# Kernel optimization log

Hardware: AMD Instinct MI355X
Metric: run time of the kernel (lower is better)

The kernel has to match this reference:

```python
import jax, jax.numpy as jnp
import numpy as np
from jax import lax

EPS = 1e-5

def setup_inputs() -> dict:
    key = jax.random.key(0)
    ks = jax.random.split(key, 9)
    B, C, O, H, W = 2, 64, 64, 192, 192
    x = jax.random.normal(ks[0], (B, C, H, W), jnp.float32)
    dw_w = jax.random.normal(ks[1], (C, 1, 3, 3), jnp.float32) * (1.0 / 3.0)
    dw_b = jax.random.normal(ks[2], (C,), jnp.float32) * 0.1
    bn_g = jnp.ones((C,), jnp.float32)
    bn_b = jnp.zeros((C,), jnp.float32)
    bn_m = jax.random.normal(ks[3], (C,), jnp.float32) * 0.1
    bn_v = jax.random.uniform(ks[4], (C,), jnp.float32, 0.5, 1.5)
    # small pointwise weights -> moderate offsets (module inits these to 0)
    pw_w = jax.random.normal(ks[5], (27, C), jnp.float32) * 0.05
    pw_b = jax.random.normal(ks[6], (27,), jnp.float32) * 0.05
    dcn_w = jax.random.normal(ks[7], (O, C, 3, 3), jnp.float32) * (1.0 / np.sqrt(C * 9))
    dcn_b = jax.random.normal(ks[8], (O,), jnp.float32) * 0.1
    return {"x": x, "dw_w": dw_w, "dw_b": dw_b, "bn_g": bn_g, "bn_b": bn_b,
            "bn_m": bn_m, "bn_v": bn_v, "pw_w": pw_w, "pw_b": pw_b,
            "dcn_w": dcn_w, "dcn_b": dcn_b}


def _dcnv2_forward(x, dw_w, dw_b, bn_g, bn_b, bn_m, bn_v, pw_w, pw_b, dcn_w, dcn_b):
    B, C, H, W = x.shape
    O = dcn_w.shape[0]
    K = 9  # 3x3 kernel positions

    # --- offset/mask head: depthwise 3x3 conv + BN(eval) + ReLU + 1x1 conv ---
    h = lax.conv_general_dilated(x, dw_w, (1, 1), ((1, 1), (1, 1)),
                                 feature_group_count=C,
                                 dimension_numbers=("NCHW", "OIHW", "NCHW"))
    h = h + dw_b[None, :, None, None]
    h = (h - bn_m[None, :, None, None]) * lax.rsqrt(bn_v + EPS)[None, :, None, None]
    h = h * bn_g[None, :, None, None] + bn_b[None, :, None, None]
    h = jax.nn.relu(h)
    om = jnp.einsum("bchw,oc->bohw", h, pw_w) + pw_b[None, :, None, None]  # [B,27,H,W]

    off = om[:, :18].reshape(B, K, 2, H, W)  # torchvision layout: (dy, dx) per kernel pos
    dy, dx = off[:, :, 0], off[:, :, 1]      # [B,K,H,W]
    mask = jax.nn.sigmoid(om[:, 18:])        # [B,K,H,W]

    # --- deformable sampling positions ---
    kk = jnp.arange(K)
    ry = (kk // 3 - 1).astype(x.dtype)[None, :, None, None]
    rx = (kk % 3 - 1).astype(x.dtype)[None, :, None, None]
    iy = jnp.arange(H, dtype=x.dtype)[None, None, :, None]
    ix = jnp.arange(W, dtype=x.dtype)[None, None, None, :]
    py = iy + ry + dy  # [B,K,H,W]
    px = ix + rx + dx

    y0 = jnp.floor(py)
    x0 = jnp.floor(px)
    wy1 = py - y0
    wx1 = px - x0
    wy0 = 1.0 - wy1
    wx0 = 1.0 - wx1

    x_flat = x.reshape(B, C, H * W)

    def gather(yi, xi):
        # zero-padded gather at integer coords yi, xi [B,K,H,W] -> [B,C,K,H,W]
        valid = (yi >= 0) & (yi < H) & (xi >= 0) & (xi < W)
        yc = jnp.clip(yi, 0, H - 1).astype(jnp.int32)
        xc = jnp.clip(xi, 0, W - 1).astype(jnp.int32)
        idx = (yc * W + xc).reshape(B, 1, K * H * W)
        v = jnp.take_along_axis(x_flat, idx, axis=2).reshape(B, C, K, H, W)
        return v * valid.astype(x.dtype)[:, None]

    val = (gather(y0, x0) * (wy0 * wx0)[:, None]
           + gather(y0, x0 + 1) * (wy0 * wx1)[:, None]
           + gather(y0 + 1, x0) * (wy1 * wx0)[:, None]
           + gather(y0 + 1, x0 + 1) * (wy1 * wx1)[:, None])  # [B,C,K,H,W]

    val = val * mask[:, None]  # DCNv2 modulation
    out = jnp.einsum("bckhw,ock->bohw", val, dcn_w.reshape(O, C, K))
    out = out + dcn_b[None, :, None, None]

    # --- InstanceNorm2d (affine=False) + ReLU ---
    mu = out.mean(axis=(2, 3), keepdims=True)
    var = out.var(axis=(2, 3), keepdims=True)
    out = (out - mu) * lax.rsqrt(var + EPS)
    return jax.nn.relu(out)


def reference(x, dw_w, dw_b, bn_g, bn_b, bn_m, bn_v, pw_w, pw_b, dcn_w, dcn_b):
    return _dcnv2_forward(x, dw_w, dw_b, bn_g, bn_b, bn_m, bn_v, pw_w, pw_b, dcn_w, dcn_b)
```

## Files before the change

kernel.cpp:

```cpp
#include <hip/hip_runtime.h>
#include <math.h>

#define H_ 192
#define W_ 192
#define HW_ 36864
#define C_ 64
#define O_ 64
#define B_ 2
#define K_ 9
#define EPS_ 1e-5f

typedef __attribute__((ext_vector_type(8))) short short8;
typedef __attribute__((ext_vector_type(4))) float f32x4;

__device__ __forceinline__ unsigned int f2bf(float f) {
  unsigned int u = __float_as_uint(f);
  u += 0x7FFFu + ((u >> 16) & 1u);
  return u >> 16;
}
__device__ __forceinline__ unsigned int pk2bf(float lo, float hi) {
  return f2bf(lo) | (f2bf(hi) << 16);
}
__device__ __forceinline__ void acc8(const uint4 u, const float g, float* v) {
  v[0] = fmaf(g, __uint_as_float(u.x << 16), v[0]);
  v[1] = fmaf(g, __uint_as_float(u.x & 0xFFFF0000u), v[1]);
  v[2] = fmaf(g, __uint_as_float(u.y << 16), v[2]);
  v[3] = fmaf(g, __uint_as_float(u.y & 0xFFFF0000u), v[3]);
  v[4] = fmaf(g, __uint_as_float(u.z << 16), v[4]);
  v[5] = fmaf(g, __uint_as_float(u.z & 0xFFFF0000u), v[5]);
  v[6] = fmaf(g, __uint_as_float(u.w << 16), v[6]);
  v[7] = fmaf(g, __uint_as_float(u.w & 0xFFFF0000u), v[7]);
}

__global__ __launch_bounds__(256) void k1_dw(const float* __restrict__ x,
                                             const float* __restrict__ dw_w,
                                             const float* __restrict__ dw_b,
                                             const float* __restrict__ bn_g,
                                             const float* __restrict__ bn_b,
                                             const float* __restrict__ bn_m,
                                             const float* __restrict__ bn_v,
                                             float* __restrict__ h) {
  const int plane = blockIdx.y;
  const int c = plane & (C_ - 1);
  const int p = blockIdx.x * 256 + threadIdx.x;
  const int y = p / W_;
  const int xx = p - y * W_;
  const float* xp = x + (size_t)plane * HW_;
  float w[9];
#pragma unroll
  for (int i = 0; i < 9; ++i) w[i] = dw_w[c * 9 + i];
  float s = 0.f;
#pragma unroll
  for (int dy = 0; dy < 3; ++dy) {
    const int yy = y + dy - 1;
    if (yy < 0 || yy >= H_) continue;
#pragma unroll
    for (int dx = 0; dx < 3; ++dx) {
      const int xc = xx + dx - 1;
      if (xc < 0 || xc >= W_) continue;
      s = fmaf(w[dy * 3 + dx], xp[yy * W_ + xc], s);
    }
  }
  const float scale = bn_g[c] * rsqrtf(bn_v[c] + EPS_);
  const float shift = fmaf(dw_b[c] - bn_m[c], scale, bn_b[c]);
  h[(size_t)plane * HW_ + p] = fmaxf(fmaf(s, scale, shift), 0.f);
}

__global__ __launch_bounds__(256) void k1b_t(const float* __restrict__ x,
                                             unsigned short* __restrict__ xR) {
  const int b = blockIdx.y;
  const int p = blockIdx.x * 256 + threadIdx.x;
  const int y = p / W_;
  const int xx = p - y * W_;
  const float* xp = x + (size_t)b * C_ * HW_ + p;
  uint4* dst = (uint4*)xR + (size_t)b * HW_ * 8;
#pragma unroll
  for (int cc = 0; cc < 8; ++cc) {
    uint4 u;
    u.x = pk2bf(xp[(size_t)(cc * 8 + 0) * HW_], xp[(size_t)(cc * 8 + 1) * HW_]);
    u.y = pk2bf(xp[(size_t)(cc * 8 + 2) * HW_], xp[(size_t)(cc * 8 + 3) * HW_]);
    u.z = pk2bf(xp[(size_t)(cc * 8 + 4) * HW_], xp[(size_t)(cc * 8 + 5) * HW_]);
    u.w = pk2bf(xp[(size_t)(cc * 8 + 6) * HW_], xp[(size_t)(cc * 8 + 7) * HW_]);
    dst[(y * 8 + cc) * W_ + xx] = u;
  }
}

__global__ __launch_bounds__(256) void k2_pw(const float* __restrict__ h,
                                             const float* __restrict__ pw_w,
                                             const float* __restrict__ pw_b,
                                             float* __restrict__ om) {
  __shared__ float wl[C_ * 28];
  const int b = blockIdx.y;
  const int p = blockIdx.x * 256 + threadIdx.x;
  for (int i = threadIdx.x; i < C_ * 28; i += 256) {
    const int c = i / 28, j = i - c * 28;
    wl[i] = (j < 27) ? pw_w[j * C_ + c] : 0.f;
  }
  __syncthreads();
  float s[27];
#pragma unroll
  for (int j = 0; j < 27; ++j) s[j] = 0.f;
  const float* hp = h + (size_t)b * C_ * HW_ + p;
  for (int c = 0; c < C_; ++c) {
    const float hv = hp[(size_t)c * HW_];
    float wv[28];
#pragma unroll
    for (int q = 0; q < 7; ++q)
      *(float4*)&wv[q * 4] = *(const float4*)&wl[c * 28 + q * 4];
#pragma unroll
    for (int j = 0; j < 27; ++j) s[j] = fmaf(hv, wv[j], s[j]);
  }
  float* op = om + (size_t)b * 27 * HW_ + p;
#pragma unroll
  for (int j = 0; j < 27; ++j) op[(size_t)j * HW_] = s[j] + pw_b[j];
}

__global__ __launch_bounds__(256) void k0_wt(const float* __restrict__ dcn_w,
                                             unsigned short* __restrict__ wT2) {
  const int i = blockIdx.x * 256 + threadIdx.x;
  const int o = i / (C_ * 9);
  const int rem = i - o * (C_ * 9);
  const int c = rem / 9;
  const int kk = rem - c * 9;
  wT2[((size_t)(kk * O_) + o) * C_ + c] = (unsigned short)f2bf(dcn_w[i]);
}

__global__ __launch_bounds__(256, 4) void k3_dcn(const unsigned short* __restrict__ xR,
                                                 const float* __restrict__ om,
                                                 const unsigned short* __restrict__ wT2,
                                                 float* __restrict__ pre,
                                                 float* __restrict__ pstats2) {
  __shared__ __align__(16) unsigned short smem[8192];
  unsigned short* wlds = smem;
  unsigned short* vlds = smem + 4096;

  const int tid = threadIdx.x;
  const int t = (blockIdx.x & 7) * 144 + (blockIdx.x >> 3);
  const int b = t / 576;
  const int p0 = (t - b * 576) * 64;
  const uint4* xr = (const uint4*)xR + (size_t)b * HW_ * 8;
  const float* omb = om + (size_t)b * 27 * HW_;

  const int pxi = tid & 63;
  const int cq = tid >> 6;
  const int lr = pxi & 15;
  const int lg = pxi >> 4;
  const int oo0 = cq * 16;

  const int p = p0 + pxi;
  const int y = p / W_;
  const int xx = p - y * W_;

  f32x4 acc[4];
#pragma unroll
  for (int j = 0; j < 4; ++j) acc[j] = (f32x4){0.f, 0.f, 0.f, 0.f};

  for (int k = 0; k < K_; ++k) {
    const uint4* wsrc = (const uint4*)(wT2 + (k << 12));
    const uint4 wv0 = wsrc[tid];
    const uint4 wv1 = wsrc[tid + 256];
    const float dyv = omb[(size_t)(2 * k) * HW_ + p];
    const float dxv = omb[(size_t)(2 * k + 1) * HW_ + p];
    float mk = omb[(size_t)(18 + k) * HW_ + p];
    mk = 1.f / (1.f + __expf(-mk));
    const int ky = k / 3;
    const int kx = k - ky * 3;
    const float py = (float)(y + ky - 1) + dyv;
    const float pxf = (float)(xx + kx - 1) + dxv;
    const float y0f = floorf(py), x0f = floorf(pxf);
    const float wy1 = py - y0f, wx1 = pxf - x0f;
    const float wy0 = 1.f - wy1, wx0 = 1.f - wx1;
    const int y0 = (int)y0f, x0i = (int)x0f;
    const int y1 = y0 + 1, x1i = x0i + 1;
    const bool vy0 = (y0 >= 0) & (y0 < H_);
    const bool vy1 = (y1 >= 0) & (y1 < H_);
    const bool vx0 = (x0i >= 0) & (x0i < W_);
    const bool vx1 = (x1i >= 0) & (x1i < W_);
    const int yc0 = min(max(y0, 0), H_ - 1), yc1 = min(max(y1, 0), H_ - 1);
    const int xc0 = min(max(x0i, 0), W_ - 1), xc1 = min(max(x1i, 0), W_ - 1);
    const float g0 = (vy0 & vx0) ? wy0 * wx0 * mk : 0.f;
    const float g1 = (vy0 & vx1) ? wy0 * wx1 * mk : 0.f;
    const float g2 = (vy1 & vx0) ? wy1 * wx0 * mk : 0.f;
    const float g3 = (vy1 & vx1) ? wy1 * wx1 * mk : 0.f;

    const int ry0 = yc0 * (8 * W_), ry1 = yc1 * (8 * W_);
    const int ca = cq * W_, cb = (cq + 4) * W_;
    const uint4 a0 = xr[ry0 + ca + xc0], b0v = xr[ry0 + cb + xc0];
    const uint4 a1 = xr[ry0 + ca + xc1], b1v = xr[ry0 + cb + xc1];
    const uint4 a2 = xr[ry1 + ca + xc0], b2v = xr[ry1 + cb + xc0];
    const uint4 a3 = xr[ry1 + ca + xc1], b3v = xr[ry1 + cb + xc1];
    float val[16];
#pragma unroll
    for (int i = 0; i < 16; ++i) val[i] = 0.f;
    acc8(a0, g0, val);  acc8(b0v, g0, val + 8);
    acc8(a1, g1, val);  acc8(b1v, g1, val + 8);
    acc8(a2, g2, val);  acc8(b2v, g2, val + 8);
    acc8(a3, g3, val);  acc8(b3v, g3, val + 8);

    __syncthreads();
    {
      const int r0 = tid >> 3, b0i = tid & 7;
      ((uint4*)wlds)[(r0 << 3) + (b0i ^ (r0 & 7))] = wv0;
      const int r1 = (tid + 256) >> 3;
      ((uint4*)wlds)[(r1 << 3) + (b0i ^ (r1 & 7))] = wv1;
    }
    {
      uint4 pka, pkb;
      pka.x = pk2bf(val[0], val[1]);
      pka.y = pk2bf(val[2], val[3]);
      pka.z = pk2bf(val[4], val[5]);
      pka.w = pk2bf(val[6], val[7]);
      pkb.x = pk2bf(val[8], val[9]);
      pkb.y = pk2bf(val[10], val[11]);
      pkb.z = pk2bf(val[12], val[13]);
      pkb.w = pk2bf(val[14], val[15]);
      const int rsw = pxi & 7;
      ((uint4*)vlds)[(pxi << 3) + (cq ^ rsw)] = pka;
      ((uint4*)vlds)[(pxi << 3) + ((cq + 4) ^ rsw)] = pkb;
    }
    __syncthreads();
#pragma unroll
    for (int ks = 0; ks < 2; ++ks) {
      const int kb = (ks << 2) + lg;
      const int ra = oo0 + lr;
      const short8 afr = *(const short8*)&((const uint4*)wlds)[(ra << 3) + (kb ^ (ra & 7))];
#pragma unroll
      for (int j = 0; j < 4; ++j) {
        const int rb = (j << 4) + lr;
        const short8 bfr = *(const short8*)&((const uint4*)vlds)[(rb << 3) + (kb ^ (rb & 7))];
        acc[j] = __builtin_amdgcn_mfma_f32_16x16x32_bf16(afr, bfr, acc[j], 0, 0, 0);
      }
    }
  }

#pragma unroll
  for (int q = 0; q < 4; ++q) {
    float s = acc[0][q] + acc[1][q] + acc[2][q] + acc[3][q];
    float s2 = fmaf(acc[0][q], acc[0][q],
               fmaf(acc[1][q], acc[1][q],
               fmaf(acc[2][q], acc[2][q], acc[3][q] * acc[3][q])));
#pragma unroll
    for (int m = 1; m < 16; m <<= 1) {
      s += __shfl_xor(s, m);
      s2 += __shfl_xor(s2, m);
    }
    if (lr == 0) {
      const int pll = oo0 + (lg << 2) + q;
      ((float2*)pstats2)[(size_t)t * 64 + pll] = make_float2(s, s2);
    }
  }

  __syncthreads();
  float* fsm = (float*)smem;
#pragma unroll
  for (int j = 0; j < 4; ++j)
#pragma unroll
    for (int q = 0; q < 4; ++q)
      fsm[(oo0 + (lg << 2) + q) * 64 + (j << 4) + lr] = acc[j][q];
  __syncthreads();
  {
    const float4* fsm4 = (const float4*)fsm;
    float* prebase = pre + (size_t)b * O_ * HW_ + p0;
#pragma unroll
    for (int i = 0; i < 4; ++i) {
      const int f = tid + (i << 8);
      const int o = f >> 4;
      const int px4 = (f & 15) << 2;
      *(float4*)&prebase[(size_t)o * HW_ + px4] = fsm4[f];
    }
  }
}

__global__ __launch_bounds__(256) void k4_fin(const float* __restrict__ pstats2,
                                              float* __restrict__ stats) {
  const int pl = blockIdx.x;
  const int b = pl >> 6, o = pl & 63;
  const float2* src = (const float2*)pstats2 + (size_t)b * 576 * 64 + o;
  float s = 0.f, s2 = 0.f;
  for (int tt = threadIdx.x; tt < 576; tt += 256) {
    const float2 v = src[(size_t)tt * 64];
    s += v.x;
    s2 += v.y;
  }
#pragma unroll
  for (int m = 1; m < 64; m <<= 1) {
    s += __shfl_xor(s, m);
    s2 += __shfl_xor(s2, m);
  }
  __shared__ float ls[4], ls2[4];
  const int wid = threadIdx.x >> 6;
  if ((threadIdx.x & 63) == 0) { ls[wid] = s; ls2[wid] = s2; }
  __syncthreads();
  if (threadIdx.x == 0) {
    const float ts = ls[0] + ls[1] + ls[2] + ls[3];
    const float ts2 = ls2[0] + ls2[1] + ls2[2] + ls2[3];
    const float inv = 1.f / (float)HW_;
    const float mu = ts * inv;
    const float var = fmaxf(fmaf(-mu, mu, ts2 * inv), 0.f);
    stats[pl * 2] = mu;
    stats[pl * 2 + 1] = rsqrtf(var + EPS_);
  }
}

__global__ __launch_bounds__(256) void k5_norm(const float* __restrict__ pre,
                                               const float* __restrict__ stats,
                                               float* __restrict__ out) {
  const int i4 = blockIdx.x * 256 + threadIdx.x;
  const int plane = i4 / 9216;
  const float mu = stats[plane * 2];
  const float rs = stats[plane * 2 + 1];
  float4 v = ((const float4*)pre)[i4];
  v.x = fmaxf((v.x - mu) * rs, 0.f);
  v.y = fmaxf((v.y - mu) * rs, 0.f);
  v.z = fmaxf((v.z - mu) * rs, 0.f);
  v.w = fmaxf((v.w - mu) * rs, 0.f);
  ((float4*)out)[i4] = v;
}

extern "C" void kernel_launch(void* const* d_in, const int* in_sizes, int n_in,
                              void* d_out, int out_size, void* d_ws, size_t ws_size,
                              hipStream_t stream) {
  const float* x = (const float*)d_in[0];
  const float* dw_w = (const float*)d_in[1];
  const float* dw_b = (const float*)d_in[2];
  const float* bn_g = (const float*)d_in[3];
  const float* bn_b = (const float*)d_in[4];
  const float* bn_m = (const float*)d_in[5];
  const float* bn_v = (const float*)d_in[6];
  const float* pw_w = (const float*)d_in[7];
  const float* pw_b = (const float*)d_in[8];
  const float* dcn_w = (const float*)d_in[9];
  float* out = (float*)d_out;

  float* ws = (float*)d_ws;
  float* h = ws;
  float* om = h + (size_t)B_ * C_ * HW_;
  unsigned short* wT2 = (unsigned short*)(om + (size_t)B_ * 27 * HW_);
  float* stats = (float*)(wT2 + (size_t)K_ * O_ * C_);
  if (ws_size < (size_t)(4718592 + 1990656 + 18432 + 256) * sizeof(float)) return;
  float* pre = h;
  unsigned short* xR = (unsigned short*)d_out;
  float* pstats2 = (float*)d_out + 2359296;

  k0_wt<<<dim3(144), dim3(256), 0, stream>>>(dcn_w, wT2);
  k1b_t<<<dim3(HW_ / 256, B_), dim3(256), 0, stream>>>(x, xR);
  k1_dw<<<dim3(HW_ / 256, B_ * C_), dim3(256), 0, stream>>>(x, dw_w, dw_b, bn_g, bn_b,
                                                            bn_m, bn_v, h);
  k2_pw<<<dim3(HW_ / 256, B_), dim3(256), 0, stream>>>(h, pw_w, pw_b, om);
  k3_dcn<<<dim3(B_ * HW_ / 64), dim3(256), 0, stream>>>(xR, om, wT2, pre, pstats2);
  k4_fin<<<dim3(B_ * O_), dim3(256), 0, stream>>>(pstats2, stats);
  k5_norm<<<dim3(B_ * O_ * HW_ / 4 / 256), dim3(256), 0, stream>>>(pre, stats, out);
}
```

Baseline: 106.7 us.

## Switch DCN sampling and MFMA to fp16, pack offsets/mask as float4

```diff
diff --git a/kernel.cpp b/kernel.cpp
--- a/kernel.cpp
+++ b/kernel.cpp
@@ -1,4 +1,5 @@
 #include <hip/hip_runtime.h>
+#include <hip/hip_fp16.h>
 #include <math.h>
 
 #define H_ 192
@@ -10,26 +11,14 @@
 #define K_ 9
 #define EPS_ 1e-5f
 
-typedef __attribute__((ext_vector_type(8))) short short8;
+typedef __attribute__((ext_vector_type(8))) _Float16 f16x8;
 typedef __attribute__((ext_vector_type(4))) float f32x4;
 
-__device__ __forceinline__ unsigned int f2bf(float f) {
-  unsigned int u = __float_as_uint(f);
-  u += 0x7FFFu + ((u >> 16) & 1u);
-  return u >> 16;
-}
-__device__ __forceinline__ unsigned int pk2bf(float lo, float hi) {
-  return f2bf(lo) | (f2bf(hi) << 16);
-}
-__device__ __forceinline__ void acc8(const uint4 u, const float g, float* v) {
-  v[0] = fmaf(g, __uint_as_float(u.x << 16), v[0]);
-  v[1] = fmaf(g, __uint_as_float(u.x & 0xFFFF0000u), v[1]);
-  v[2] = fmaf(g, __uint_as_float(u.y << 16), v[2]);
-  v[3] = fmaf(g, __uint_as_float(u.y & 0xFFFF0000u), v[3]);
-  v[4] = fmaf(g, __uint_as_float(u.z << 16), v[4]);
-  v[5] = fmaf(g, __uint_as_float(u.z & 0xFFFF0000u), v[5]);
-  v[6] = fmaf(g, __uint_as_float(u.w << 16), v[6]);
-  v[7] = fmaf(g, __uint_as_float(u.w & 0xFFFF0000u), v[7]);
+union U16B { uint4 u; __half2 h[4]; };
+
+__device__ __forceinline__ unsigned int pkh(float lo, float hi) {
+  return (unsigned int)__half_as_ushort(__float2half(lo)) |
+         ((unsigned int)__half_as_ushort(__float2half(hi)) << 16);
 }
 
 __global__ __launch_bounds__(256) void k1_dw(const float* __restrict__ x,
@@ -77,10 +66,10 @@
 #pragma unroll
   for (int cc = 0; cc < 8; ++cc) {
     uint4 u;
-    u.x = pk2bf(xp[(size_t)(cc * 8 + 0) * HW_], xp[(size_t)(cc * 8 + 1) * HW_]);
-    u.y = pk2bf(xp[(size_t)(cc * 8 + 2) * HW_], xp[(size_t)(cc * 8 + 3) * HW_]);
-    u.z = pk2bf(xp[(size_t)(cc * 8 + 4) * HW_], xp[(size_t)(cc * 8 + 5) * HW_]);
-    u.w = pk2bf(xp[(size_t)(cc * 8 + 6) * HW_], xp[(size_t)(cc * 8 + 7) * HW_]);
+    u.x = pkh(xp[(size_t)(cc * 8 + 0) * HW_], xp[(size_t)(cc * 8 + 1) * HW_]);
+    u.y = pkh(xp[(size_t)(cc * 8 + 2) * HW_], xp[(size_t)(cc * 8 + 3) * HW_]);
+    u.z = pkh(xp[(size_t)(cc * 8 + 4) * HW_], xp[(size_t)(cc * 8 + 5) * HW_]);
+    u.w = pkh(xp[(size_t)(cc * 8 + 6) * HW_], xp[(size_t)(cc * 8 + 7) * HW_]);
     dst[(y * 8 + cc) * W_ + xx] = u;
   }
 }
@@ -88,31 +77,49 @@
 __global__ __launch_bounds__(256) void k2_pw(const float* __restrict__ h,
                                              const float* __restrict__ pw_w,
                                              const float* __restrict__ pw_b,
-                                             float* __restrict__ om) {
+                                             float4* __restrict__ om4) {
   __shared__ float wl[C_ * 28];
   const int b = blockIdx.y;
-  const int p = blockIdx.x * 256 + threadIdx.x;
+  const int p0 = blockIdx.x * 512 + threadIdx.x;
   for (int i = threadIdx.x; i < C_ * 28; i += 256) {
     const int c = i / 28, j = i - c * 28;
     wl[i] = (j < 27) ? pw_w[j * C_ + c] : 0.f;
   }
   __syncthreads();
-  float s[27];
-#pragma unroll
-  for (int j = 0; j < 27; ++j) s[j] = 0.f;
-  const float* hp = h + (size_t)b * C_ * HW_ + p;
+  float sa[27], sb[27];
+#pragma unroll
+  for (int j = 0; j < 27; ++j) { sa[j] = 0.f; sb[j] = 0.f; }
+  const float* hp = h + (size_t)b * C_ * HW_ + p0;
   for (int c = 0; c < C_; ++c) {
-    const float hv = hp[(size_t)c * HW_];
+    const float hv0 = hp[(size_t)c * HW_];
+    const float hv1 = hp[(size_t)c * HW_ + 256];
     float wv[28];
 #pragma unroll
     for (int q = 0; q < 7; ++q)
       *(float4*)&wv[q * 4] = *(const float4*)&wl[c * 28 + q * 4];
 #pragma unroll
-    for (int j = 0; j < 27; ++j) s[j] = fmaf(hv, wv[j], s[j]);
-  }
-  float* op = om + (size_t)b * 27 * HW_ + p;
-#pragma unroll
-  for (int j = 0; j < 27; ++j) op[(size_t)j * HW_] = s[j] + pw_b[j];
+    for (int j = 0; j < 27; ++j) {
+      sa[j] = fmaf(hv0, wv[j], sa[j]);
+      sb[j] = fmaf(hv1, wv[j], sb[j]);
+    }
+  }
+  float4* op = om4 + (size_t)b * 9 * HW_;
+#pragma unroll
+  for (int k = 0; k < 9; ++k) {
+    const float ry = (float)(k / 3 - 1), rx = (float)(k % 3 - 1);
+    const float b0 = pw_b[2 * k], b1 = pw_b[2 * k + 1], b2 = pw_b[18 + k];
+    float4 va, vb;
+    va.x = sa[2 * k] + b0 + ry;
+    va.y = sa[2 * k + 1] + b1 + rx;
+    va.z = 1.f / (1.f + __expf(-(sa[18 + k] + b2)));
+    va.w = 0.f;
+    vb.x = sb[2 * k] + b0 + ry;
+    vb.y = sb[2 * k + 1] + b1 + rx;
+    vb.z = 1.f / (1.f + __expf(-(sb[18 + k] + b2)));
+    vb.w = 0.f;
+    op[(size_t)k * HW_ + p0] = va;
+    op[(size_t)k * HW_ + p0 + 256] = vb;
+  }
 }
 
 __global__ __launch_bounds__(256) void k0_wt(const float* __restrict__ dcn_w,
@@ -122,11 +129,11 @@
   const int rem = i - o * (C_ * 9);
   const int c = rem / 9;
   const int kk = rem - c * 9;
-  wT2[((size_t)(kk * O_) + o) * C_ + c] = (unsigned short)f2bf(dcn_w[i]);
+  wT2[((size_t)(kk * O_) + o) * C_ + c] = __half_as_ushort(__float2half(dcn_w[i]));
 }
 
 __global__ __launch_bounds__(256, 4) void k3_dcn(const unsigned short* __restrict__ xR,
-                                                 const float* __restrict__ om,
+                                                 const float4* __restrict__ om4,
                                                  const unsigned short* __restrict__ wT2,
                                                  float* __restrict__ pre,
                                                  float* __restrict__ pstats2) {
@@ -139,7 +146,7 @@
   const int b = t / 576;
   const int p0 = (t - b * 576) * 64;
   const uint4* xr = (const uint4*)xR + (size_t)b * HW_ * 8;
-  const float* omb = om + (size_t)b * 27 * HW_;
+  const float4* omb = om4 + (size_t)b * 9 * HW_;
 
   const int pxi = tid & 63;
   const int cq = tid >> 6;
@@ -159,14 +166,10 @@
     const uint4* wsrc = (const uint4*)(wT2 + (k << 12));
     const uint4 wv0 = wsrc[tid];
     const uint4 wv1 = wsrc[tid + 256];
-    const float dyv = omb[(size_t)(2 * k) * HW_ + p];
-    const float dxv = omb[(size_t)(2 * k + 1) * HW_ + p];
-    float mk = omb[(size_t)(18 + k) * HW_ + p];
-    mk = 1.f / (1.f + __expf(-mk));
-    const int ky = k / 3;
-    const int kx = k - ky * 3;
-    const float py = (float)(y + ky - 1) + dyv;
-    const float pxf = (float)(xx + kx - 1) + dxv;
+    const float4 od = omb[(size_t)k * HW_ + p];
+    const float py = (float)y + od.x;
+    const float pxf = (float)xx + od.y;
+    const float mk = od.z;
     const float y0f = floorf(py), x0f = floorf(pxf);
     const float wy1 = py - y0f, wx1 = pxf - x0f;
     const float wy0 = 1.f - wy1, wx0 = 1.f - wx1;
@@ -185,17 +188,30 @@
 
     const int ry0 = yc0 * (8 * W_), ry1 = yc1 * (8 * W_);
     const int ca = cq * W_, cb = (cq + 4) * W_;
-    const uint4 a0 = xr[ry0 + ca + xc0], b0v = xr[ry0 + cb + xc0];
-    const uint4 a1 = xr[ry0 + ca + xc1], b1v = xr[ry0 + cb + xc1];
-    const uint4 a2 = xr[ry1 + ca + xc0], b2v = xr[ry1 + cb + xc0];
-    const uint4 a3 = xr[ry1 + ca + xc1], b3v = xr[ry1 + cb + xc1];
-    float val[16];
-#pragma unroll
-    for (int i = 0; i < 16; ++i) val[i] = 0.f;
-    acc8(a0, g0, val);  acc8(b0v, g0, val + 8);
-    acc8(a1, g1, val);  acc8(b1v, g1, val + 8);
-    acc8(a2, g2, val);  acc8(b2v, g2, val + 8);
-    acc8(a3, g3, val);  acc8(b3v, g3, val + 8);
+    U16B a0, a1, a2, a3, b0v, b1v, b2v, b3v;
+    a0.u = xr[ry0 + ca + xc0];  b0v.u = xr[ry0 + cb + xc0];
+    a1.u = xr[ry0 + ca + xc1];  b1v.u = xr[ry0 + cb + xc1];
+    a2.u = xr[ry1 + ca + xc0];  b2v.u = xr[ry1 + cb + xc0];
+    a3.u = xr[ry1 + ca + xc1];  b3v.u = xr[ry1 + cb + xc1];
+
+    const __half2 g0h = __float2half2_rn(g0);
+    const __half2 g1h = __float2half2_rn(g1);
+    const __half2 g2h = __float2half2_rn(g2);
+    const __half2 g3h = __float2half2_rn(g3);
+    U16B va, vb;
+    va.u = make_uint4(0, 0, 0, 0);
+    vb.u = make_uint4(0, 0, 0, 0);
+#pragma unroll
+    for (int i = 0; i < 4; ++i) {
+      va.h[i] = __hfma2(a0.h[i], g0h, va.h[i]);
+      vb.h[i] = __hfma2(b0v.h[i], g0h, vb.h[i]);
+      va.h[i] = __hfma2(a1.h[i], g1h, va.h[i]);
+      vb.h[i] = __hfma2(b1v.h[i], g1h, vb.h[i]);
+      va.h[i] = __hfma2(a2.h[i], g2h, va.h[i]);
+      vb.h[i] = __hfma2(b2v.h[i], g2h, vb.h[i]);
+      va.h[i] = __hfma2(a3.h[i], g3h, va.h[i]);
+      vb.h[i] = __hfma2(b3v.h[i], g3h, vb.h[i]);
+    }
 
     __syncthreads();
     {
@@ -205,30 +221,21 @@
       ((uint4*)wlds)[(r1 << 3) + (b0i ^ (r1 & 7))] = wv1;
     }
     {
-      uint4 pka, pkb;
-      pka.x = pk2bf(val[0], val[1]);
-      pka.y = pk2bf(val[2], val[3]);
-      pka.z = pk2bf(val[4], val[5]);
-      pka.w = pk2bf(val[6], val[7]);
-      pkb.x = pk2bf(val[8], val[9]);
-      pkb.y = pk2bf(val[10], val[11]);
-      pkb.z = pk2bf(val[12], val[13]);
-      pkb.w = pk2bf(val[14], val[15]);
       const int rsw = pxi & 7;
-      ((uint4*)vlds)[(pxi << 3) + (cq ^ rsw)] = pka;
-      ((uint4*)vlds)[(pxi << 3) + ((cq + 4) ^ rsw)] = pkb;
+      ((uint4*)vlds)[(pxi << 3) + (cq ^ rsw)] = va.u;
+      ((uint4*)vlds)[(pxi << 3) + ((cq + 4) ^ rsw)] = vb.u;
     }
     __syncthreads();
 #pragma unroll
     for (int ks = 0; ks < 2; ++ks) {
       const int kb = (ks << 2) + lg;
       const int ra = oo0 + lr;
-      const short8 afr = *(const short8*)&((const uint4*)wlds)[(ra << 3) + (kb ^ (ra & 7))];
+      const f16x8 afr = *(const f16x8*)&((const uint4*)wlds)[(ra << 3) + (kb ^ (ra & 7))];
 #pragma unroll
       for (int j = 0; j < 4; ++j) {
         const int rb = (j << 4) + lr;
-        const short8 bfr = *(const short8*)&((const uint4*)vlds)[(rb << 3) + (kb ^ (rb & 7))];
-        acc[j] = __builtin_amdgcn_mfma_f32_16x16x32_bf16(afr, bfr, acc[j], 0, 0, 0);
+        const f16x8 bfr = *(const f16x8*)&((const uint4*)vlds)[(rb << 3) + (kb ^ (rb & 7))];
+        acc[j] = __builtin_amdgcn_mfma_f32_16x16x32_f16(afr, bfr, acc[j], 0, 0, 0);
       }
     }
   }
@@ -334,10 +341,10 @@
 
   float* ws = (float*)d_ws;
   float* h = ws;
-  float* om = h + (size_t)B_ * C_ * HW_;
-  unsigned short* wT2 = (unsigned short*)(om + (size_t)B_ * 27 * HW_);
+  float4* om4 = (float4*)(h + (size_t)B_ * C_ * HW_);
+  unsigned short* wT2 = (unsigned short*)((float*)om4 + (size_t)B_ * 9 * HW_ * 4);
   float* stats = (float*)(wT2 + (size_t)K_ * O_ * C_);
-  if (ws_size < (size_t)(4718592 + 1990656 + 18432 + 256) * sizeof(float)) return;
+  if (ws_size < (size_t)(4718592 + 2654208 + 18432 + 256) * sizeof(float)) return;
   float* pre = h;
   unsigned short* xR = (unsigned short*)d_out;
   float* pstats2 = (float*)d_out + 2359296;
@@ -346,8 +353,8 @@
   k1b_t<<<dim3(HW_ / 256, B_), dim3(256), 0, stream>>>(x, xR);
   k1_dw<<<dim3(HW_ / 256, B_ * C_), dim3(256), 0, stream>>>(x, dw_w, dw_b, bn_g, bn_b,
                                                             bn_m, bn_v, h);
-  k2_pw<<<dim3(HW_ / 256, B_), dim3(256), 0, stream>>>(h, pw_w, pw_b, om);
-  k3_dcn<<<dim3(B_ * HW_ / 64), dim3(256), 0, stream>>>(xR, om, wT2, pre, pstats2);
+  k2_pw<<<dim3(HW_ / 512, B_), dim3(256), 0, stream>>>(h, pw_w, pw_b, om4);
+  k3_dcn<<<dim3(B_ * HW_ / 64), dim3(256), 0, stream>>>(xR, om4, wT2, pre, pstats2);
   k4_fin<<<dim3(B_ * O_), dim3(256), 0, stream>>>(pstats2, stats);
   k5_norm<<<dim3(B_ * O_ * HW_ / 4 / 256), dim3(256), 0, stream>>>(pre, stats, out);
 }
```

Result: slower. 113.3 us (+6.2%).
